# Performance work log

Measured on AMD Instinct MI355X. Metric: run time of the kernel, lower is better.

The kernel has to match this reference:

```python
import jax, jax.numpy as jnp
import numpy as np

NUM_HEADS = 5
TEMP = 0.3
NEG_FILL = -1e-7  # note: NOT -inf; masked entries still contribute ~exp(0) to softmax, faithful to torch code


def setup_inputs() -> dict:
    key = jax.random.key(0)
    k1, k2, k3, k4, k5 = jax.random.split(key, 5)
    B, N, F_IN, F_OUT = 8, 1024, 320, 320
    h = jax.random.normal(k1, (B, N, F_IN), dtype=jnp.float32)
    Wqk = jax.random.normal(k2, (F_IN, 2 * F_IN), dtype=jnp.float32) * (1.0 / np.sqrt(F_IN))
    bqk = jax.random.normal(k3, (2 * F_IN,), dtype=jnp.float32) * 0.01
    weight = jax.random.normal(k4, (F_IN, F_OUT), dtype=jnp.float32) * (1.0 / np.sqrt(F_OUT))
    bias = jax.random.normal(k5, (F_OUT,), dtype=jnp.float32) * 0.01
    return {"h": h, "Wqk": Wqk, "bqk": bqk, "weight": weight, "bias": bias}


def reference(h, Wqk, bqk, weight, bias):
    B, N, F = h.shape
    H = NUM_HEADS
    D = F // H
    # linear -> [b, n, 2F]; einops 'b n (h d qk)' => reshape (b, n, h, d, 2)
    qk = (h @ Wqk + bqk).reshape(B, N, H, D, 2)
    q = jnp.transpose(qk[..., 0], (0, 2, 1, 3))  # b h n d
    k = jnp.transpose(qk[..., 1], (0, 2, 1, 3))  # b h n d
    scale = D ** -0.5
    dots = jnp.einsum('bhqd,bhkd->bhqk', q, k) * scale  # b h n n
    at = dots.sum(axis=1)  # b n n  (sum over heads)
    # sort-based threshold: keep values >= descending-sorted value at index N//6
    thr = jax.lax.top_k(at, N // 6 + 1)[0][..., -1]  # b n
    adj = jnp.where(at < thr[:, :, None], jnp.asarray(NEG_FILL, at.dtype), at)
    attn = jax.nn.softmax(adj / TEMP, axis=2)  # b n n
    out_feature = jnp.einsum('bij,bjd->bid', attn, h)  # values = raw input h
    return out_feature @ weight + bias
```

## Files before the change

### kernel.cpp

```cpp
#include <hip/hip_runtime.h>
#include <hip/hip_fp16.h>


typedef __attribute__((ext_vector_type(8))) _Float16 half8;
typedef __attribute__((ext_vector_type(4))) float f32x4;

__device__ __forceinline__ void stage_tile(const __half* g, __half* lds,
                                           int nrow16, int ld, int wave, int lane) {
    const int r = lane >> 2;
    const int c = ((lane & 3) ^ ((lane >> 3) & 3)) * 8;
    for (int i = wave; i < nrow16; i += 4) {
        const __half* src = g + (long)(i * 16 + r) * ld + c;
        __builtin_amdgcn_global_load_lds(
            (const __attribute__((address_space(1))) unsigned int*)src,
            (__attribute__((address_space(3))) unsigned int*)(lds + i * 512),
            16, 0, 0);
    }
}

__device__ __forceinline__ void stage_tile8(const __half* g, __half* lds,
                                            int nrow16, int ld, int wave, int lane) {
    const int r = lane >> 2;
    const int c = ((lane & 3) ^ ((lane >> 3) & 3)) * 8;
    for (int i = wave; i < nrow16; i += 8) {
        const __half* src = g + (long)(i * 16 + r) * ld + c;
        __builtin_amdgcn_global_load_lds(
            (const __attribute__((address_space(1))) unsigned int*)src,
            (__attribute__((address_space(3))) unsigned int*)(lds + i * 512),
            16, 0, 0);
    }
}

template <int EPI>
__device__ __forceinline__ void gemm_body(
    const __half* __restrict__ A, const __half* __restrict__ B,
    void* __restrict__ C, void* __restrict__ C2, const float* __restrict__ bias,
    int lda, int ldb, int ldc, int bx, int by, __half* smem)
{
    constexpr int BUF = 16384;
    const int tid  = threadIdx.x;
    const int lane = tid & 63;
    const int wave = tid >> 6;
    const int wm   = wave >> 1;
    const int wn   = wave & 1;

    const __half* Ab = A + (long)by * 128 * lda;
    const __half* Bb = B + (long)bx * 128 * ldb;

    f32x4 acc[4][4];
    #pragma unroll
    for (int i = 0; i < 4; ++i)
        #pragma unroll
        for (int j = 0; j < 4; ++j) acc[i][j] = (f32x4){0.f, 0.f, 0.f, 0.f};

    const int lrow = lane & 15;
    const int quad = lane >> 4;
    const int swz = (quad ^ ((lrow >> 1) & 3)) * 8;

    #pragma unroll
    for (int c = 0; c < 2; ++c) {
        stage_tile(Ab + c * 32, smem + c * 4096, 8, lda, wave, lane);
        stage_tile(Bb + c * 32, smem + 8192 + c * 4096, 8, ldb, wave, lane);
    }

    for (int it = 0; it < 5; ++it) {
        __syncthreads();
        if (it + 1 < 5) {
            __half* nb = smem + ((it + 1) & 1) * BUF;
            const int k1 = (it + 1) * 64;
            #pragma unroll
            for (int c = 0; c < 2; ++c) {
                stage_tile(Ab + k1 + c * 32, nb + c * 4096, 8, lda, wave, lane);
                stage_tile(Bb + k1 + c * 32, nb + 8192 + c * 4096, 8, ldb, wave, lane);
            }
        }
        const __half* buf = smem + (it & 1) * BUF;
        #pragma unroll
        for (int c = 0; c < 2; ++c) {
            const __half* pA = buf + c * 4096 + (wm * 64 + lrow) * 32 + swz;
            const __half* pB = buf + 8192 + c * 4096 + (wn * 64 + lrow) * 32 + swz;
            half8 ah[4], bh[4];
            #pragma unroll
            for (int mt = 0; mt < 4; ++mt) ah[mt] = *(const half8*)(pA + mt * 512);
            #pragma unroll
            for (int nt = 0; nt < 4; ++nt) bh[nt] = *(const half8*)(pB + nt * 512);
            #pragma unroll
            for (int mt = 0; mt < 4; ++mt)
                #pragma unroll
                for (int nt = 0; nt < 4; ++nt)
                    acc[mt][nt] = __builtin_amdgcn_mfma_f32_16x16x32_f16(
                        ah[mt], bh[nt], acc[mt][nt], 0, 0, 0);
        }
    }

    const int row_base = by * 128 + wm * 64;
    const int col_base = bx * 128 + wn * 64;
    #pragma unroll
    for (int mt = 0; mt < 4; ++mt)
        #pragma unroll
        for (int nt = 0; nt < 4; ++nt)
            #pragma unroll
            for (int r = 0; r < 4; ++r) {
                const int row = row_base + mt * 16 + quad * 4 + r;
                const int col = col_base + nt * 16 + lrow;
                const float v = acc[mt][nt][r];
                if (EPI == 1) {
                    const float val = v + bias[col];
                    const long idx = (long)row * 320 + (col >> 1);
                    if (col & 1) ((__half*)C2)[idx] = __float2half(val);
                    else         ((__half*)C)[idx]  = __float2half(val);
                } else {
                    ((__half*)C)[(long)row * ldc + col] = __float2half(v);
                }
            }
}

__global__ __launch_bounds__(256) void g1_combined(
    const __half* __restrict__ h16, const __half* __restrict__ wTp,
    const __half* __restrict__ WqkT, __half* __restrict__ hWT,
    __half* __restrict__ Q, __half* __restrict__ Kb,
    const float* __restrict__ bqk)
{
    __shared__ __half smem[2 * 16384];
    const int bx = blockIdx.x;
    if (bx < 192) {
        gemm_body<2>(wTp, h16, hWT, nullptr, nullptr,
                     320, 320, 8192, bx % 64, bx / 64, smem);
    } else {
        const int b = bx - 192;
        gemm_body<1>(h16, WqkT, Q, Kb, bqk,
                     320, 320, 320, b % 5, b / 5, smem);
    }
}

__global__ __launch_bounds__(256) void prep_all(
    const float* __restrict__ h, ushort4* __restrict__ h16,
    const float* __restrict__ Wqk, __half* __restrict__ WqkT,
    const float* __restrict__ weight, __half* __restrict__ wTp)
{
    const int bx = blockIdx.x;
    if (bx < 2560) {
        const int i = bx * 256 + threadIdx.x;
        const float4 v = ((const float4*)h)[i];
        ushort4 o;
        o.x = __half_as_ushort(__float2half(v.x));
        o.y = __half_as_ushort(__float2half(v.y));
        o.z = __half_as_ushort(__float2half(v.z));
        o.w = __half_as_ushort(__float2half(v.w));
        h16[i] = o;
        return;
    }
    __shared__ float t[32][33];
    const float* src;
    __half* dst;
    int ldS, ldT, c0, r0;
    if (bx < 2760) {
        const int b = bx - 2560;
        src = Wqk; dst = WqkT; ldS = 640; ldT = 320;
        c0 = (b % 20) * 32; r0 = (b / 20) * 32;
    } else {
        const int b = bx - 2760;
        src = weight; dst = wTp; ldS = 320; ldT = 320;
        c0 = (b % 10) * 32; r0 = (b / 10) * 32;
    }
    const int lx = threadIdx.x & 31, ly = threadIdx.x >> 5;
    #pragma unroll
    for (int i = 0; i < 4; ++i)
        t[ly + 8 * i][lx] = src[(long)(r0 + ly + 8 * i) * ldS + c0 + lx];
    __syncthreads();
    #pragma unroll
    for (int i = 0; i < 4; ++i)
        dst[(long)(c0 + ly + 8 * i) * ldT + r0 + lx] = __float2half(t[lx][ly + 8 * i]);
}

__global__ __launch_bounds__(512, 2) void fused_attn(
    const __half* __restrict__ Q, const __half* __restrict__ Kmat,
    const __half* __restrict__ hWT, const float* __restrict__ bias,
    float* __restrict__ out)
{
    __shared__ __half smem[75776];
    __half* const P = smem;
    __half* const X = smem + 32768;

    const int tid  = threadIdx.x;
    const int lane = tid & 63;
    const int wave = tid >> 6;
    const int lrow = lane & 15;
    const int quad = lane >> 4;
    const int swz  = (quad ^ ((lrow >> 1) & 3)) * 8;

    const int b  = blockIdx.x & 7;
    const int r0 = (blockIdx.x >> 3) * 32;

    const __half* Qb = Q    + (long)(b * 1024 + r0) * 320;
    const __half* Kb = Kmat + (long)b * 327680;
    const __half* Wb = hWT  + (long)b * 1024;

    __half* const Xq = X;
    __half* const XB = X + 10240;

    #pragma unroll
    for (int c = 0; c < 10; ++c)
        stage_tile8(Qb + c * 32, Xq + c * 1024, 2, 320, wave, lane);
    stage_tile8(Kb, XB, 32, 320, wave, lane);

    f32x4 acc[2][4];
    #pragma unroll
    for (int i = 0; i < 2; ++i)
        #pragma unroll
        for (int j = 0; j < 4; ++j) acc[i][j] = (f32x4){0.f, 0.f, 0.f, 0.f};

    for (int r = 0; r < 20; ++r) {
        __syncthreads();
        if (r + 1 < 20) {
            const int rn = r + 1;
            stage_tile8(Kb + (long)(rn / 10) * 512 * 320 + (rn % 10) * 32,
                        XB + (rn & 1) * 16384, 32, 320, wave, lane);
        }
        const int ks = r % 10;
        const __half* Bt = XB + (r & 1) * 16384;
        const __half* At = Xq + ks * 1024;
        half8 ah[2], bh[4];
        #pragma unroll
        for (int mi = 0; mi < 2; ++mi)
            ah[mi] = *(const half8*)(At + (mi * 16 + lrow) * 32 + swz);
        #pragma unroll
        for (int nf = 0; nf < 4; ++nf)
            bh[nf] = *(const half8*)(Bt + (wave * 64 + nf * 16 + lrow) * 32 + swz);
        #pragma unroll
        for (int mi = 0; mi < 2; ++mi)
            #pragma unroll
            for (int nf = 0; nf < 4; ++nf)
                acc[mi][nf] = __builtin_amdgcn_mfma_f32_16x16x32_f16(
                    ah[mi], bh[nf], acc[mi][nf], 0, 0, 0);
        if (ks == 9) {
            const int cb = (r / 10) * 512 + wave * 64;
            #pragma unroll
            for (int mi = 0; mi < 2; ++mi)
                #pragma unroll
                for (int nf = 0; nf < 4; ++nf)
                    #pragma unroll
                    for (int rr = 0; rr < 4; ++rr) {
                        const int row = mi * 16 + quad * 4 + rr;
                        const int col = cb + nf * 16 + lrow;
                        P[((row << 10) + col) ^ ((row & 7) << 3)] =
                            __float2half(0.125f * acc[mi][nf][rr]);
                        acc[mi][nf][rr] = 0.f;
                    }
        }
    }

    __syncthreads();
    stage_tile8(Wb,       X,         20, 8192, wave, lane);
    stage_tile8(Wb + 512, X + 20480, 20, 8192, wave, lane);

    int (*const hist)[256] = (int(*)[256])(X + 10240);

    for (int j = 0; j < 4; ++j) {
        const int row  = wave * 4 + j;
        const int key8 = (row & 7) << 3;
        const int base = (row << 10) + lane * 16;

        unsigned short vs[16];
        *(uint4*)&vs[0] = *(const uint4*)&P[base ^ key8];
        *(uint4*)&vs[8] = *(const uint4*)&P[(base + 8) ^ key8];

        unsigned key[16];
        #pragma unroll
        for (int i = 0; i < 16; ++i) {
            const unsigned u = vs[i];
            key[i] = (u & 0x8000u) ? ((~u) & 0xFFFFu) : (u | 0x8000u);
        }

        unsigned prefix = 0, pmask = 0;
        int kk = 171;

        #pragma unroll
        for (int pass = 0; pass < 2; ++pass) {
            const int shift = 8 - 8 * pass;
            *(int4*)&hist[wave][lane * 4] = make_int4(0, 0, 0, 0);
            __syncthreads();
            #pragma unroll
            for (int i = 0; i < 16; ++i) {
                if ((key[i] & pmask) == prefix)
                    atomicAdd(&hist[wave][(key[i] >> shift) & 255], 1);
            }
            __syncthreads();
            const int4 hh = *(const int4*)&hist[wave][lane * 4];
            const int s = hh.x + hh.y + hh.z + hh.w;
            int suf = s;
            #pragma unroll
            for (int off = 1; off < 64; off <<= 1) {
                const int o = __shfl_down(suf, off);
                if (lane + off < 64) suf += o;
            }
            const int cgt3 = suf - s;
            const int cgt2 = cgt3 + hh.w;
            const int cgt1 = cgt2 + hh.z;
            const int cgt0 = cgt1 + hh.y;
            int pick = 0x7FFFFFFF;
            if (cgt3 < kk && kk <= cgt3 + hh.w) pick = ((4 * lane + 3) << 16) | (kk - cgt3);
            if (cgt2 < kk && kk <= cgt2 + hh.z) pick = ((4 * lane + 2) << 16) | (kk - cgt2);
            if (cgt1 < kk && kk <= cgt1 + hh.y) pick = ((4 * lane + 1) << 16) | (kk - cgt1);
            if (cgt0 < kk && kk <= cgt0 + hh.x) pick = ((4 * lane + 0) << 16) | (kk - cgt0);
            #pragma unroll
            for (int off = 32; off > 0; off >>= 1) pick = min(pick, __shfl_xor(pick, off));
            const unsigned digit = (unsigned)(pick >> 16);
            kk = pick & 0xFFFF;
            prefix |= digit << shift;
            pmask  |= 0xFFu << shift;
            if (pass == 0) __syncthreads();
        }

        const unsigned short tu = (prefix & 0x8000u) ? (unsigned short)(prefix & 0x7FFFu)
                                                     : (unsigned short)((~prefix) & 0xFFFFu);
        const float thr = __half2float(__ushort_as_half(tu));

        float lg[16];
        float mx = -3.4e38f;
        #pragma unroll
        for (int i = 0; i < 16; ++i) {
            const float v = __half2float(__ushort_as_half(vs[i]));
            const float a = (v < thr) ? -1e-7f : v;
            lg[i] = a * (1.0f / 0.3f);
            mx = fmaxf(mx, lg[i]);
        }
        #pragma unroll
        for (int off = 32; off > 0; off >>= 1) mx = fmaxf(mx, __shfl_xor(mx, off));

        float e[16];
        float sum = 0.f;
        #pragma unroll
        for (int i = 0; i < 16; ++i) { e[i] = __expf(lg[i] - mx); sum += e[i]; }
        #pragma unroll
        for (int off = 32; off > 0; off >>= 1) sum += __shfl_xor(sum, off);
        const float inv = 1.0f / sum;

        unsigned short os[16];
        #pragma unroll
        for (int i = 0; i < 16; ++i) os[i] = __half_as_ushort(__float2half(e[i] * inv));
        *(uint4*)&P[base ^ key8]       = *(const uint4*)&os[0];
        *(uint4*)&P[(base + 8) ^ key8] = *(const uint4*)&os[8];
    }

    const int q4 = wave & 3;
    const int kh = wave >> 2;

    f32x4 acc4[2][5];
    #pragma unroll
    for (int i = 0; i < 2; ++i)
        #pragma unroll
        for (int j = 0; j < 5; ++j) acc4[i][j] = (f32x4){0.f, 0.f, 0.f, 0.f};

    for (int r = 0; r < 16; ++r) {
        __syncthreads();
        if (r + 1 < 16) {
            stage_tile8(Wb + (r + 1) * 32,       X + ((r + 1) & 1) * 10240,
                        20, 8192, wave, lane);
            stage_tile8(Wb + 512 + (r + 1) * 32, X + 20480 + ((r + 1) & 1) * 10240,
                        20, 8192, wave, lane);
        }
        const __half* T = X + kh * 20480 + (r & 1) * 10240;
        const int kk = kh * 512 + r * 32 + quad * 8;
        half8 ah[2], bh[5];
        #pragma unroll
        for (int mi = 0; mi < 2; ++mi) {
            const int row = mi * 16 + lrow;
            ah[mi] = *(const half8*)&P[((row << 10) + kk) ^ ((row & 7) << 3)];
        }
        #pragma unroll
        for (int nf = 0; nf < 5; ++nf)
            bh[nf] = *(const half8*)(T + (q4 * 80 + nf * 16 + lrow) * 32 + swz);
        #pragma unroll
        for (int mi = 0; mi < 2; ++mi)
            #pragma unroll
            for (int nf = 0; nf < 5; ++nf)
                acc4[mi][nf] = __builtin_amdgcn_mfma_f32_16x16x32_f16(
                    ah[mi], bh[nf], acc4[mi][nf], 0, 0, 0);
    }

    __syncthreads();
    float* const red = (float*)X;
    if (kh == 1) {
        #pragma unroll
        for (int mi = 0; mi < 2; ++mi)
            #pragma unroll
            for (int nf = 0; nf < 5; ++nf)
                #pragma unroll
                for (int rr = 0; rr < 4; ++rr)
                    red[(mi * 16 + quad * 4 + rr) * 320 + q4 * 80 + nf * 16 + lrow] =
                        acc4[mi][nf][rr];
    }
    __syncthreads();
    if (kh == 0) {
        #pragma unroll
        for (int mi = 0; mi < 2; ++mi)
            #pragma unroll
            for (int nf = 0; nf < 5; ++nf)
                #pragma unroll
                for (int rr = 0; rr < 4; ++rr) {
                    const int row = mi * 16 + quad * 4 + rr;
                    const int col = q4 * 80 + nf * 16 + lrow;
                    out[(long)(b * 1024 + r0 + row) * 320 + col] =
                        acc4[mi][nf][rr] + red[row * 320 + col] + bias[col];
                }
    }
}

extern "C" void kernel_launch(void* const* d_in, const int* in_sizes, int n_in,
                              void* d_out, int out_size, void* d_ws, size_t ws_size,
                              hipStream_t stream) {
    (void)in_sizes; (void)n_in; (void)out_size; (void)ws_size;

    const float* h      = (const float*)d_in[0];
    const float* Wqk    = (const float*)d_in[1];
    const float* bqk    = (const float*)d_in[2];
    const float* weight = (const float*)d_in[3];
    const float* bias   = (const float*)d_in[4];
    float* out = (float*)d_out;

    char* p = (char*)d_ws;
    __half* h16  = (__half*)p; p += 2621440L * 2;
    __half* Q    = (__half*)p; p += 2621440L * 2;
    __half* Kb   = (__half*)p; p += 2621440L * 2;
    __half* WqkT = (__half*)p; p += 640L * 320 * 2;
    __half* wTp  = (__half*)p; p += 384L * 320 * 2;
    __half* hWT  = (__half*)p; p += 384L * 8192 * 2;

    prep_all<<<2860, 256, 0, stream>>>(h, (ushort4*)h16, Wqk, WqkT, weight, wTp);

    g1_combined<<<512, 256, 0, stream>>>(h16, wTp, WqkT, hWT, Q, Kb, bqk);

    fused_attn<<<256, 512, 0, stream>>>(Q, Kb, hWT, bias, out);
}
```

Before: 137.2 us.

## Load Q/K and hW operands directly from global into registers, dropping LDS staging

The fused attention kernel no longer stages Q, K and the hW^T tiles through LDS with double-buffered async copies. Q fragments are held in registers, and K and W fragments are loaded straight from global memory, which relies on L2 for reuse. This shrinks shared memory to the P tile plus the histogram, which could allow more resident blocks and removes per-step barriers. The cost is uncoalesced 16-byte global loads with no prefetch overlap, plus higher register pressure from holding Q.

```diff
diff --git a/kernel.cpp b/kernel.cpp
--- a/kernel.cpp
+++ b/kernel.cpp
@@ -10,19 +10,6 @@
     const int r = lane >> 2;
     const int c = ((lane & 3) ^ ((lane >> 3) & 3)) * 8;
     for (int i = wave; i < nrow16; i += 4) {
-        const __half* src = g + (long)(i * 16 + r) * ld + c;
-        __builtin_amdgcn_global_load_lds(
-            (const __attribute__((address_space(1))) unsigned int*)src,
-            (__attribute__((address_space(3))) unsigned int*)(lds + i * 512),
-            16, 0, 0);
-    }
-}
-
-__device__ __forceinline__ void stage_tile8(const __half* g, __half* lds,
-                                            int nrow16, int ld, int wave, int lane) {
-    const int r = lane >> 2;
-    const int c = ((lane & 3) ^ ((lane >> 3) & 3)) * 8;
-    for (int i = wave; i < nrow16; i += 8) {
         const __half* src = g + (long)(i * 16 + r) * ld + c;
         __builtin_amdgcn_global_load_lds(
             (const __attribute__((address_space(1))) unsigned int*)src,
@@ -178,16 +165,14 @@
     const __half* __restrict__ hWT, const float* __restrict__ bias,
     float* __restrict__ out)
 {
-    __shared__ __half smem[75776];
-    __half* const P = smem;
-    __half* const X = smem + 32768;
+    __shared__ __half P[32768];
+    __shared__ int hist[8][256];
 
     const int tid  = threadIdx.x;
     const int lane = tid & 63;
     const int wave = tid >> 6;
     const int lrow = lane & 15;
     const int quad = lane >> 4;
-    const int swz  = (quad ^ ((lrow >> 1) & 3)) * 8;
 
     const int b  = blockIdx.x & 7;
     const int r0 = (blockIdx.x >> 3) * 32;
@@ -196,65 +181,49 @@
     const __half* Kb = Kmat + (long)b * 327680;
     const __half* Wb = hWT  + (long)b * 1024;
 
-    __half* const Xq = X;
-    __half* const XB = X + 10240;
-
-    #pragma unroll
-    for (int c = 0; c < 10; ++c)
-        stage_tile8(Qb + c * 32, Xq + c * 1024, 2, 320, wave, lane);
-    stage_tile8(Kb, XB, 32, 320, wave, lane);
-
-    f32x4 acc[2][4];
-    #pragma unroll
-    for (int i = 0; i < 2; ++i)
-        #pragma unroll
-        for (int j = 0; j < 4; ++j) acc[i][j] = (f32x4){0.f, 0.f, 0.f, 0.f};
-
-    for (int r = 0; r < 20; ++r) {
-        __syncthreads();
-        if (r + 1 < 20) {
-            const int rn = r + 1;
-            stage_tile8(Kb + (long)(rn / 10) * 512 * 320 + (rn % 10) * 32,
-                        XB + (rn & 1) * 16384, 32, 320, wave, lane);
-        }
-        const int ks = r % 10;
-        const __half* Bt = XB + (r & 1) * 16384;
-        const __half* At = Xq + ks * 1024;
-        half8 ah[2], bh[4];
+    half8 qreg[10][2];
+    #pragma unroll
+    for (int kc = 0; kc < 10; ++kc)
         #pragma unroll
         for (int mi = 0; mi < 2; ++mi)
-            ah[mi] = *(const half8*)(At + (mi * 16 + lrow) * 32 + swz);
-        #pragma unroll
-        for (int nf = 0; nf < 4; ++nf)
-            bh[nf] = *(const half8*)(Bt + (wave * 64 + nf * 16 + lrow) * 32 + swz);
-        #pragma unroll
-        for (int mi = 0; mi < 2; ++mi)
-            #pragma unroll
-            for (int nf = 0; nf < 4; ++nf)
-                acc[mi][nf] = __builtin_amdgcn_mfma_f32_16x16x32_f16(
-                    ah[mi], bh[nf], acc[mi][nf], 0, 0, 0);
-        if (ks == 9) {
-            const int cb = (r / 10) * 512 + wave * 64;
+            qreg[kc][mi] = *(const half8*)(Qb + (long)(mi * 16 + lrow) * 320
+                                           + kc * 32 + quad * 8);
+
+    const __half* Kw = Kb + (long)(wave * 128 + lrow) * 320 + quad * 8;
+    #pragma unroll
+    for (int cg = 0; cg < 2; ++cg) {
+        f32x4 acc[4][2];
+        #pragma unroll
+        for (int i = 0; i < 4; ++i)
+            #pragma unroll
+            for (int j = 0; j < 2; ++j) acc[i][j] = (f32x4){0.f, 0.f, 0.f, 0.f};
+        #pragma unroll
+        for (int kc = 0; kc < 10; ++kc) {
+            half8 bh[4];
+            #pragma unroll
+            for (int cb = 0; cb < 4; ++cb)
+                bh[cb] = *(const half8*)(Kw + (long)(cg * 64 + cb * 16) * 320
+                                         + kc * 32);
+            #pragma unroll
+            for (int cb = 0; cb < 4; ++cb)
+                #pragma unroll
+                for (int mi = 0; mi < 2; ++mi)
+                    acc[cb][mi] = __builtin_amdgcn_mfma_f32_16x16x32_f16(
+                        qreg[kc][mi], bh[cb], acc[cb][mi], 0, 0, 0);
+        }
+        #pragma unroll
+        for (int cb = 0; cb < 4; ++cb)
             #pragma unroll
             for (int mi = 0; mi < 2; ++mi)
                 #pragma unroll
-                for (int nf = 0; nf < 4; ++nf)
-                    #pragma unroll
-                    for (int rr = 0; rr < 4; ++rr) {
-                        const int row = mi * 16 + quad * 4 + rr;
-                        const int col = cb + nf * 16 + lrow;
-                        P[((row << 10) + col) ^ ((row & 7) << 3)] =
-                            __float2half(0.125f * acc[mi][nf][rr]);
-                        acc[mi][nf][rr] = 0.f;
-                    }
-        }
-    }
-
+                for (int rr = 0; rr < 4; ++rr) {
+                    const int row = mi * 16 + quad * 4 + rr;
+                    const int col = wave * 128 + cg * 64 + cb * 16 + lrow;
+                    P[((row << 10) + col) ^ ((row & 7) << 3)] =
+                        __float2half(0.125f * acc[cb][mi][rr]);
+                }
+    }
     __syncthreads();
-    stage_tile8(Wb,       X,         20, 8192, wave, lane);
-    stage_tile8(Wb + 512, X + 20480, 20, 8192, wave, lane);
-
-    int (*const hist)[256] = (int(*)[256])(X + 10240);
 
     for (int j = 0; j < 4; ++j) {
         const int row  = wave * 4 + j;
@@ -342,67 +311,63 @@
         *(uint4*)&P[base ^ key8]       = *(const uint4*)&os[0];
         *(uint4*)&P[(base + 8) ^ key8] = *(const uint4*)&os[8];
     }
+    __syncthreads();
 
     const int q4 = wave & 3;
     const int kh = wave >> 2;
 
-    f32x4 acc4[2][5];
-    #pragma unroll
-    for (int i = 0; i < 2; ++i)
-        #pragma unroll
-        for (int j = 0; j < 5; ++j) acc4[i][j] = (f32x4){0.f, 0.f, 0.f, 0.f};
-
-    for (int r = 0; r < 16; ++r) {
-        __syncthreads();
-        if (r + 1 < 16) {
-            stage_tile8(Wb + (r + 1) * 32,       X + ((r + 1) & 1) * 10240,
-                        20, 8192, wave, lane);
-            stage_tile8(Wb + 512 + (r + 1) * 32, X + 20480 + ((r + 1) & 1) * 10240,
-                        20, 8192, wave, lane);
-        }
-        const __half* T = X + kh * 20480 + (r & 1) * 10240;
-        const int kk = kh * 512 + r * 32 + quad * 8;
-        half8 ah[2], bh[5];
+    f32x4 acc4[5][2];
+    #pragma unroll
+    for (int i = 0; i < 5; ++i)
+        #pragma unroll
+        for (int j = 0; j < 2; ++j) acc4[i][j] = (f32x4){0.f, 0.f, 0.f, 0.f};
+
+    const __half* Wq = Wb + (long)(q4 * 80 + lrow) * 8192 + kh * 512 + quad * 8;
+    #pragma unroll 4
+    for (int t = 0; t < 16; ++t) {
+        half8 bh[5];
+        #pragma unroll
+        for (int cf = 0; cf < 5; ++cf)
+            bh[cf] = *(const half8*)(Wq + (long)cf * 16 * 8192 + t * 32);
+        const int kk = kh * 512 + t * 32 + quad * 8;
+        half8 ah[2];
         #pragma unroll
         for (int mi = 0; mi < 2; ++mi) {
             const int row = mi * 16 + lrow;
             ah[mi] = *(const half8*)&P[((row << 10) + kk) ^ ((row & 7) << 3)];
         }
         #pragma unroll
-        for (int nf = 0; nf < 5; ++nf)
-            bh[nf] = *(const half8*)(T + (q4 * 80 + nf * 16 + lrow) * 32 + swz);
-        #pragma unroll
-        for (int mi = 0; mi < 2; ++mi)
-            #pragma unroll
-            for (int nf = 0; nf < 5; ++nf)
-                acc4[mi][nf] = __builtin_amdgcn_mfma_f32_16x16x32_f16(
-                    ah[mi], bh[nf], acc4[mi][nf], 0, 0, 0);
+        for (int cf = 0; cf < 5; ++cf)
+            #pragma unroll
+            for (int mi = 0; mi < 2; ++mi)
+                acc4[cf][mi] = __builtin_amdgcn_mfma_f32_16x16x32_f16(
+                    ah[mi], bh[cf], acc4[cf][mi], 0, 0, 0);
     }
 
     __syncthreads();
-    float* const red = (float*)X;
+    float* const red = (float*)P;
     if (kh == 1) {
         #pragma unroll
-        for (int mi = 0; mi < 2; ++mi)
-            #pragma unroll
-            for (int nf = 0; nf < 5; ++nf)
+        for (int cf = 0; cf < 5; ++cf)
+            #pragma unroll
+            for (int mi = 0; mi < 2; ++mi)
                 #pragma unroll
                 for (int rr = 0; rr < 4; ++rr)
-                    red[(mi * 16 + quad * 4 + rr) * 320 + q4 * 80 + nf * 16 + lrow] =
-                        acc4[mi][nf][rr];
+                    red[(mi * 16 + quad * 4 + rr) * 320 + q4 * 80 + cf * 16 + lrow] =
+                        acc4[cf][mi][rr];
     }
     __syncthreads();
     if (kh == 0) {
         #pragma unroll
-        for (int mi = 0; mi < 2; ++mi)
-            #pragma unroll
-            for (int nf = 0; nf < 5; ++nf)
+        for (int cf = 0; cf < 5; ++cf)
+            #pragma unroll
+            for (int mi = 0; mi < 2; ++mi)
                 #pragma unroll
                 for (int rr = 0; rr < 4; ++rr) {
                     const int row = mi * 16 + quad * 4 + rr;
-                    const int col = q4 * 80 + nf * 16 + lrow;
+                    const int col = q4 * 80 + cf * 16 + lrow;
                     out[(long)(b * 1024 + r0 + row) * 320 + col] =
-                        acc4[mi][nf][rr] + red[row * 320 + col] + bias[col];
+                        acc4[cf][mi][rr] + red[row * 320 + col] + bias[col];
                 }
     }
 }
```

Measured after the change: 146.9 us. 1.07x slower.
